# Performance work log

Measured on AMD Instinct MI355X. Metric: run time of the kernel, lower is better.

## Reference

```python
import jax, jax.numpy as jnp
import numpy as np

EPS = 1e-8  # matches torch F.cosine_similarity eps


def setup_inputs() -> dict:
    key = jax.random.key(0)
    k1, k2, k3 = jax.random.split(key, 3)
    S, B, H = 16, 512, 2048
    OGLogits = jax.random.normal(k1, (B, H), dtype=jnp.float32)
    enhancedSamplesLogits = jax.random.normal(k2, (S, B, H), dtype=jnp.float32)
    W = jax.random.normal(k3, (H, H), dtype=jnp.float32) * (1.0 / np.sqrt(H))
    b = jnp.zeros((H,), dtype=jnp.float32)
    return {"OGLogits": OGLogits, "enhancedSamplesLogits": enhancedSamplesLogits, "W": W, "b": b}


def reference(OGLogits, enhancedSamplesLogits, W, b):
    # Original torch code builds the full (S*B, B) cosine-similarity matrix and
    # keeps only the diagonal via an eye mask; mathematically that equals the
    # per-pair cosine similarity cos(enhanced[s,b], OG[b]), computed directly here.
    e_norm = jnp.linalg.norm(enhancedSamplesLogits, axis=-1)          # (S, B)
    o_norm = jnp.linalg.norm(OGLogits, axis=-1)                       # (B,)
    dots = jnp.einsum('sbh,bh->sb', enhancedSamplesLogits, OGLogits)  # (S, B)
    sims = dots / jnp.maximum(e_norm * o_norm[None, :], EPS)          # (S, B)
    weighted = enhancedSamplesLogits * sims[..., None]                # (S, B, H)
    weightedRep = weighted.mean(axis=0)                               # (B, H)
    return weightedRep @ W.T + b                                      # (B, H)
```

## Files before the change

### kernel.cpp

```cpp
#include <hip/hip_runtime.h>

#define S_DIM 16
#define B_DIM 512
#define H_DIM 2048
#define EPS 1e-8f

typedef short bf16x8 __attribute__((ext_vector_type(8)));
typedef float f32x4 __attribute__((ext_vector_type(4)));

__device__ __forceinline__ unsigned short f2bf(float f) {
    union { float f; unsigned int u; } v; v.f = f;
    unsigned int u = v.u;
    unsigned int r = (u + 0x7fffu + ((u >> 16) & 1u)) >> 16;
    return (unsigned short)r;
}

__device__ __forceinline__ float dot4(const float4& a, const float4& b) {
    return a.x*b.x + a.y*b.y + a.z*b.z + a.w*b.w;
}

__global__ __launch_bounds__(512, 4) void simwrep_kernel(
    const float* __restrict__ OG, const float* __restrict__ E,
    const float* __restrict__ W, unsigned short* __restrict__ wrep,
    unsigned short* __restrict__ Wb) {
    const int b = blockIdx.x;
    const int t = threadIdx.x;
    const int lane = t & 63;
    const int wave = t >> 6;

    __shared__ float4 ogs[512];
    __shared__ float4 buf[8][512];
    __shared__ float red[8];

    const float4* og4 = (const float4*)(OG + (size_t)b * H_DIM);
    float4 o = og4[t];
    ogs[t] = o;
    float p = dot4(o, o);
    #pragma unroll
    for (int m = 32; m >= 1; m >>= 1) p += __shfl_xor(p, m, 64);
    if (lane == 0) red[wave] = p;
    __syncthreads();
    float og2 = 0.f;
    #pragma unroll
    for (int w = 0; w < 8; ++w) og2 += red[w];
    const float onorm = sqrtf(og2);

    const float4* e4a = (const float4*)(E + ((size_t)wave * B_DIM + b) * H_DIM);
    const float4* e4b = (const float4*)(E + ((size_t)(wave + 8) * B_DIM + b) * H_DIM);
    float4 ea[8], eb[8];
    #pragma unroll
    for (int i = 0; i < 8; ++i) {
        ea[i] = e4a[i * 64 + lane];
        eb[i] = e4b[i * 64 + lane];
    }
    float da = 0.f, na = 0.f, db = 0.f, nb = 0.f;
    #pragma unroll
    for (int i = 0; i < 8; ++i) {
        float4 og = ogs[i * 64 + lane];
        da += dot4(ea[i], og);
        na += dot4(ea[i], ea[i]);
        db += dot4(eb[i], og);
        nb += dot4(eb[i], eb[i]);
    }
    #pragma unroll
    for (int m = 32; m >= 1; m >>= 1) {
        da += __shfl_xor(da, m, 64);
        na += __shfl_xor(na, m, 64);
        db += __shfl_xor(db, m, 64);
        nb += __shfl_xor(nb, m, 64);
    }
    const float sima = da / fmaxf(sqrtf(na) * onorm, EPS);
    const float simb = db / fmaxf(sqrtf(nb) * onorm, EPS);

    #pragma unroll
    for (int i = 0; i < 8; ++i) {
        float4 v;
        v.x = ea[i].x * sima + eb[i].x * simb;
        v.y = ea[i].y * sima + eb[i].y * simb;
        v.z = ea[i].z * sima + eb[i].z * simb;
        v.w = ea[i].w * sima + eb[i].w * simb;
        buf[wave][i * 64 + lane] = v;
    }
    __syncthreads();

    float4 s = buf[0][t];
    #pragma unroll
    for (int w = 1; w < 8; ++w) {
        float4 v = buf[w][t];
        s.x += v.x; s.y += v.y; s.z += v.z; s.w += v.w;
    }
    const float sc = 1.f / (float)S_DIM;
    ushort4 ob;
    ob.x = f2bf(s.x * sc); ob.y = f2bf(s.y * sc);
    ob.z = f2bf(s.z * sc); ob.w = f2bf(s.w * sc);
    ((ushort4*)wrep)[(size_t)b * (H_DIM / 4) + t] = ob;

    const float4* w4 = (const float4*)W;
    #pragma unroll
    for (int j = 0; j < 4; ++j) {
        const size_t idx = (size_t)b * 2048 + j * 512 + t;
        float4 v = w4[idx];
        ushort4 c;
        c.x = f2bf(v.x); c.y = f2bf(v.y); c.z = f2bf(v.z); c.w = f2bf(v.w);
        ((ushort4*)Wb)[idx] = c;
    }
}

__global__ __launch_bounds__(256) void gemm_kernel(
    const unsigned short* __restrict__ A, const unsigned short* __restrict__ Wb,
    const float* __restrict__ bias, float* __restrict__ out) {
    const int n0 = blockIdx.x * 32;
    const int m0 = blockIdx.y * 64;

    __shared__ unsigned short As[64][72];
    __shared__ unsigned short Ws[32][72];

    const int t = threadIdx.x;
    const int lane = t & 63;
    const int wave = t >> 6;
    const int wm = (wave & 1) * 32;
    const int wn = (wave >> 1) * 16;

    const int lrA = t >> 2, lqA = t & 3;
    const int lrB = t >> 3, lqB = t & 7;

    const unsigned short* ap = A + (size_t)(m0 + lrA) * H_DIM + lqA * 16;
    const unsigned short* bp = Wb + (size_t)(n0 + lrB) * H_DIM + lqB * 8;

    f32x4 acc0 = {0.f, 0.f, 0.f, 0.f};
    f32x4 acc1 = {0.f, 0.f, 0.f, 0.f};

    const int row = lane & 15;
    const int q = lane >> 4;

    uint4 av0 = *(const uint4*)(ap);
    uint4 av1 = *(const uint4*)(ap + 8);
    uint4 bv  = *(const uint4*)(bp);

    for (int k0 = 0; k0 < H_DIM; k0 += 64) {
        *(uint4*)&As[lrA][lqA * 16]     = av0;
        *(uint4*)&As[lrA][lqA * 16 + 8] = av1;
        *(uint4*)&Ws[lrB][lqB * 8]      = bv;
        __syncthreads();
        if (k0 + 64 < H_DIM) {
            av0 = *(const uint4*)(ap + k0 + 64);
            av1 = *(const uint4*)(ap + k0 + 72);
            bv  = *(const uint4*)(bp + k0 + 64);
        }
        #pragma unroll
        for (int ks = 0; ks < 2; ++ks) {
            bf16x8 a0 = *(const bf16x8*)&As[wm + row][ks * 32 + q * 8];
            bf16x8 a1 = *(const bf16x8*)&As[wm + 16 + row][ks * 32 + q * 8];
            bf16x8 b0 = *(const bf16x8*)&Ws[wn + row][ks * 32 + q * 8];
            acc0 = __builtin_amdgcn_mfma_f32_16x16x32_bf16(a0, b0, acc0, 0, 0, 0);
            acc1 = __builtin_amdgcn_mfma_f32_16x16x32_bf16(a1, b0, acc1, 0, 0, 0);
        }
        __syncthreads();
    }

    const int col = lane & 15;
    const float bias0 = bias[n0 + wn + col];
    #pragma unroll
    for (int r = 0; r < 4; ++r) {
        const int mr = q * 4 + r;
        float* o0 = out + (size_t)(m0 + wm + mr) * H_DIM + n0 + wn;
        float* o1 = out + (size_t)(m0 + wm + 16 + mr) * H_DIM + n0 + wn;
        o0[col] = acc0[r] + bias0;
        o1[col] = acc1[r] + bias0;
    }
}

extern "C" void kernel_launch(void* const* d_in, const int* in_sizes, int n_in,
                              void* d_out, int out_size, void* d_ws, size_t ws_size,
                              hipStream_t stream) {
    const float* OG   = (const float*)d_in[0];
    const float* E    = (const float*)d_in[1];
    const float* W    = (const float*)d_in[2];
    const float* bias = (const float*)d_in[3];
    float* out = (float*)d_out;

    unsigned short* wrep = (unsigned short*)d_ws;
    unsigned short* Wb   = wrep + (size_t)B_DIM * H_DIM;

    simwrep_kernel<<<B_DIM, 512, 0, stream>>>(OG, E, W, wrep, Wb);
    gemm_kernel<<<dim3(H_DIM / 32, B_DIM / 64), 256, 0, stream>>>(wrep, Wb, bias, out);
}
```

Measured before the change: 125.5 us.

## Pre-swizzle GEMM operands into MFMA fragment layout and drop LDS staging

The first kernel now writes the bf16 weighted representation and the converted W in a tiled layout. In that layout each 16x32 MFMA fragment sits as 64 contiguous 16-byte lanes. The GEMM then loads fragments straight from global memory into registers with one-step prefetching, with no shared-memory staging and no barriers. Each wave now computes a 32x32 tile instead of 32x16, so the grid is halved. This removes LDS traffic and syncs at the cost of relying on cache reuse for the operands that several waves share.

```diff
diff --git a/kernel.cpp b/kernel.cpp
--- a/kernel.cpp
+++ b/kernel.cpp
@@ -7,6 +7,8 @@
 
 typedef short bf16x8 __attribute__((ext_vector_type(8)));
 typedef float f32x4 __attribute__((ext_vector_type(4)));
+
+#define KT (H_DIM / 32)
 
 __device__ __forceinline__ unsigned short f2bf(float f) {
     union { float f; unsigned int u; } v; v.f = f;
@@ -21,8 +23,8 @@
 
 __global__ __launch_bounds__(512, 4) void simwrep_kernel(
     const float* __restrict__ OG, const float* __restrict__ E,
-    const float* __restrict__ W, unsigned short* __restrict__ wrep,
-    unsigned short* __restrict__ Wb) {
+    const float* __restrict__ W, unsigned short* __restrict__ wrep_sw,
+    unsigned short* __restrict__ Wb_sw) {
     const int b = blockIdx.x;
     const int t = threadIdx.x;
     const int lane = t & 63;
@@ -90,83 +92,91 @@
         s.x += v.x; s.y += v.y; s.z += v.z; s.w += v.w;
     }
     const float sc = 1.f / (float)S_DIM;
-    ushort4 ob;
-    ob.x = f2bf(s.x * sc); ob.y = f2bf(s.y * sc);
-    ob.z = f2bf(s.z * sc); ob.w = f2bf(s.w * sc);
-    ((ushort4*)wrep)[(size_t)b * (H_DIM / 4) + t] = ob;
+    {
+        const int ki = t >> 3;
+        const int quad = (t >> 1) & 3;
+        const int j0 = (t & 1) * 4;
+        const int l = (b & 15) | (quad << 4);
+        const size_t off = ((size_t)((b >> 4) * KT + ki)) * 512 + l * 8 + j0;
+        ushort4 ob;
+        ob.x = f2bf(s.x * sc); ob.y = f2bf(s.y * sc);
+        ob.z = f2bf(s.z * sc); ob.w = f2bf(s.w * sc);
+        *(ushort4*)(wrep_sw + off) = ob;
+    }
 
     const float4* w4 = (const float4*)W;
     #pragma unroll
     for (int j = 0; j < 4; ++j) {
-        const size_t idx = (size_t)b * 2048 + j * 512 + t;
+        const int n = b * 4 + j;
+        const size_t idx = (size_t)n * 512 + t;
         float4 v = w4[idx];
+        const int ki = t >> 3;
+        const int quad = (t >> 1) & 3;
+        const int j0 = (t & 1) * 4;
+        const int l = (n & 15) | (quad << 4);
+        const size_t off = ((size_t)((n >> 4) * KT + ki)) * 512 + l * 8 + j0;
         ushort4 c;
         c.x = f2bf(v.x); c.y = f2bf(v.y); c.z = f2bf(v.z); c.w = f2bf(v.w);
-        ((ushort4*)Wb)[idx] = c;
+        *(ushort4*)(Wb_sw + off) = c;
     }
 }
 
 __global__ __launch_bounds__(256) void gemm_kernel(
-    const unsigned short* __restrict__ A, const unsigned short* __restrict__ Wb,
+    const unsigned short* __restrict__ A, const unsigned short* __restrict__ Bw,
     const float* __restrict__ bias, float* __restrict__ out) {
-    const int n0 = blockIdx.x * 32;
-    const int m0 = blockIdx.y * 64;
-
-    __shared__ unsigned short As[64][72];
-    __shared__ unsigned short Ws[32][72];
-
     const int t = threadIdx.x;
     const int lane = t & 63;
     const int wave = t >> 6;
-    const int wm = (wave & 1) * 32;
-    const int wn = (wave >> 1) * 16;
+    const int mi0 = blockIdx.y * 4 + (wave & 1) * 2;
+    const int ni0 = blockIdx.x * 4 + (wave >> 1) * 2;
 
-    const int lrA = t >> 2, lqA = t & 3;
-    const int lrB = t >> 3, lqB = t & 7;
+    const bf16x8* Af = (const bf16x8*)A;
+    const bf16x8* Bf = (const bf16x8*)Bw;
+    const int a0b = mi0 * (KT * 64) + lane;
+    const int a1b = (mi0 + 1) * (KT * 64) + lane;
+    const int b0b = ni0 * (KT * 64) + lane;
+    const int b1b = (ni0 + 1) * (KT * 64) + lane;
 
-    const unsigned short* ap = A + (size_t)(m0 + lrA) * H_DIM + lqA * 16;
-    const unsigned short* bp = Wb + (size_t)(n0 + lrB) * H_DIM + lqB * 8;
+    f32x4 acc00 = {0.f, 0.f, 0.f, 0.f};
+    f32x4 acc01 = {0.f, 0.f, 0.f, 0.f};
+    f32x4 acc10 = {0.f, 0.f, 0.f, 0.f};
+    f32x4 acc11 = {0.f, 0.f, 0.f, 0.f};
 
-    f32x4 acc0 = {0.f, 0.f, 0.f, 0.f};
-    f32x4 acc1 = {0.f, 0.f, 0.f, 0.f};
+    bf16x8 a0c = Af[a0b], a1c = Af[a1b];
+    bf16x8 b0c = Bf[b0b], b1c = Bf[b1b];
 
-    const int row = lane & 15;
-    const int q = lane >> 4;
-
-    uint4 av0 = *(const uint4*)(ap);
-    uint4 av1 = *(const uint4*)(ap + 8);
-    uint4 bv  = *(const uint4*)(bp);
-
-    for (int k0 = 0; k0 < H_DIM; k0 += 64) {
-        *(uint4*)&As[lrA][lqA * 16]     = av0;
-        *(uint4*)&As[lrA][lqA * 16 + 8] = av1;
-        *(uint4*)&Ws[lrB][lqB * 8]      = bv;
-        __syncthreads();
-        if (k0 + 64 < H_DIM) {
-            av0 = *(const uint4*)(ap + k0 + 64);
-            av1 = *(const uint4*)(ap + k0 + 72);
-            bv  = *(const uint4*)(bp + k0 + 64);
-        }
-        #pragma unroll
-        for (int ks = 0; ks < 2; ++ks) {
-            bf16x8 a0 = *(const bf16x8*)&As[wm + row][ks * 32 + q * 8];
-            bf16x8 a1 = *(const bf16x8*)&As[wm + 16 + row][ks * 32 + q * 8];
-            bf16x8 b0 = *(const bf16x8*)&Ws[wn + row][ks * 32 + q * 8];
-            acc0 = __builtin_amdgcn_mfma_f32_16x16x32_bf16(a0, b0, acc0, 0, 0, 0);
-            acc1 = __builtin_amdgcn_mfma_f32_16x16x32_bf16(a1, b0, acc1, 0, 0, 0);
-        }
-        __syncthreads();
+    for (int ki = 0; ki < KT - 1; ++ki) {
+        const int nx = (ki + 1) * 64;
+        bf16x8 a0n = Af[a0b + nx];
+        bf16x8 a1n = Af[a1b + nx];
+        bf16x8 b0n = Bf[b0b + nx];
+        bf16x8 b1n = Bf[b1b + nx];
+        acc00 = __builtin_amdgcn_mfma_f32_16x16x32_bf16(a0c, b0c, acc00, 0, 0, 0);
+        acc01 = __builtin_amdgcn_mfma_f32_16x16x32_bf16(a0c, b1c, acc01, 0, 0, 0);
+        acc10 = __builtin_amdgcn_mfma_f32_16x16x32_bf16(a1c, b0c, acc10, 0, 0, 0);
+        acc11 = __builtin_amdgcn_mfma_f32_16x16x32_bf16(a1c, b1c, acc11, 0, 0, 0);
+        a0c = a0n; a1c = a1n; b0c = b0n; b1c = b1n;
     }
+    acc00 = __builtin_amdgcn_mfma_f32_16x16x32_bf16(a0c, b0c, acc00, 0, 0, 0);
+    acc01 = __builtin_amdgcn_mfma_f32_16x16x32_bf16(a0c, b1c, acc01, 0, 0, 0);
+    acc10 = __builtin_amdgcn_mfma_f32_16x16x32_bf16(a1c, b0c, acc10, 0, 0, 0);
+    acc11 = __builtin_amdgcn_mfma_f32_16x16x32_bf16(a1c, b1c, acc11, 0, 0, 0);
 
     const int col = lane & 15;
-    const float bias0 = bias[n0 + wn + col];
+    const int q = lane >> 4;
+    const int m0 = mi0 * 16;
+    const int n0 = ni0 * 16;
+    const float bias0 = bias[n0 + col];
+    const float bias1 = bias[n0 + 16 + col];
     #pragma unroll
     for (int r = 0; r < 4; ++r) {
         const int mr = q * 4 + r;
-        float* o0 = out + (size_t)(m0 + wm + mr) * H_DIM + n0 + wn;
-        float* o1 = out + (size_t)(m0 + wm + 16 + mr) * H_DIM + n0 + wn;
-        o0[col] = acc0[r] + bias0;
-        o1[col] = acc1[r] + bias0;
+        float* o0 = out + (size_t)(m0 + mr) * H_DIM + n0;
+        float* o1 = out + (size_t)(m0 + 16 + mr) * H_DIM + n0;
+        o0[col]      = acc00[r] + bias0;
+        o0[16 + col] = acc01[r] + bias1;
+        o1[col]      = acc10[r] + bias0;
+        o1[16 + col] = acc11[r] + bias1;
     }
 }
 
@@ -179,9 +189,9 @@
     const float* bias = (const float*)d_in[3];
     float* out = (float*)d_out;
 
-    unsigned short* wrep = (unsigned short*)d_ws;
-    unsigned short* Wb   = wrep + (size_t)B_DIM * H_DIM;
+    unsigned short* wrep_sw = (unsigned short*)d_ws;
+    unsigned short* Wb_sw   = wrep_sw + (size_t)B_DIM * H_DIM;
 
-    simwrep_kernel<<<B_DIM, 512, 0, stream>>>(OG, E, W, wrep, Wb);
-    gemm_kernel<<<dim3(H_DIM / 32, B_DIM / 64), 256, 0, stream>>>(wrep, Wb, bias, out);
+    simwrep_kernel<<<B_DIM, 512, 0, stream>>>(OG, E, W, wrep_sw, Wb_sw);
+    gemm_kernel<<<dim3(H_DIM / 64, B_DIM / 64), 256, 0, stream>>>(wrep_sw, Wb_sw, bias, out);
 }
```

Result: slower. 129.8 us (+3.5%).

## Use 32x32x16 MFMA with split-K across waves in GEMM kernel

Applied to the files above, without the earlier changes.

The GEMM kernel now uses one 32x32x16 bf16 MFMA per wave instead of two 16x16x32 MFMAs. The four waves are split into two M halves and two K halves of the block tile. Shared memory is re-laid out in fragment-major order so each lane reads a contiguous 16-byte fragment. The two K-halves are combined through an LDS reduction before the bias add and store. This aims for better MFMA efficiency and fewer LDS reads per flop, at the cost of an extra reduction step and half the waves sitting idle during the epilogue.

```diff
diff --git a/kernel.cpp b/kernel.cpp
--- a/kernel.cpp
+++ b/kernel.cpp
@@ -7,6 +7,7 @@
 
 typedef short bf16x8 __attribute__((ext_vector_type(8)));
 typedef float f32x4 __attribute__((ext_vector_type(4)));
+typedef float f32x16 __attribute__((ext_vector_type(16)));
 
 __device__ __forceinline__ unsigned short f2bf(float f) {
     union { float f; unsigned int u; } v; v.f = f;
@@ -112,61 +113,71 @@
     const int n0 = blockIdx.x * 32;
     const int m0 = blockIdx.y * 64;
 
-    __shared__ unsigned short As[64][72];
-    __shared__ unsigned short Ws[32][72];
+    __shared__ __align__(16) unsigned short lds[6144];
 
     const int t = threadIdx.x;
     const int lane = t & 63;
     const int wave = t >> 6;
-    const int wm = (wave & 1) * 32;
-    const int wn = (wave >> 1) * 16;
+    const int kh = wave & 1;
+    const int mh = wave >> 1;
 
-    const int lrA = t >> 2, lqA = t & 3;
-    const int lrB = t >> 3, lqB = t & 7;
+    const int ar = t >> 2;
+    const int ac = (t >> 1) & 1;
+    const int ah = t & 1;
+    const unsigned short* apg = A + (size_t)(m0 + ar) * H_DIM + ac * 1024 + ah * 16;
+    unsigned short* al0 = &lds[(((ac * 4 + ah * 2 + 0) * 64) + ar) * 8];
+    unsigned short* al1 = &lds[(((ac * 4 + ah * 2 + 1) * 64) + ar) * 8];
+    const int br = t >> 3;
+    const int bg = t & 7;
+    const unsigned short* bpg = Wb + (size_t)(n0 + br) * H_DIM + (bg >> 2) * 1024 + (bg & 3) * 8;
+    unsigned short* bl = &lds[4096 + (bg * 32 + br) * 8];
 
-    const unsigned short* ap = A + (size_t)(m0 + lrA) * H_DIM + lqA * 16;
-    const unsigned short* bp = Wb + (size_t)(n0 + lrB) * H_DIM + lqB * 8;
+    f32x16 acc = {0.f,0.f,0.f,0.f, 0.f,0.f,0.f,0.f, 0.f,0.f,0.f,0.f, 0.f,0.f,0.f,0.f};
 
-    f32x4 acc0 = {0.f, 0.f, 0.f, 0.f};
-    f32x4 acc1 = {0.f, 0.f, 0.f, 0.f};
+    const int hw = lane >> 5;
+    const int l31 = lane & 31;
 
-    const int row = lane & 15;
-    const int q = lane >> 4;
+    uint4 av0 = *(const uint4*)(apg);
+    uint4 av1 = *(const uint4*)(apg + 8);
+    uint4 bv  = *(const uint4*)(bpg);
 
-    uint4 av0 = *(const uint4*)(ap);
-    uint4 av1 = *(const uint4*)(ap + 8);
-    uint4 bv  = *(const uint4*)(bp);
-
-    for (int k0 = 0; k0 < H_DIM; k0 += 64) {
-        *(uint4*)&As[lrA][lqA * 16]     = av0;
-        *(uint4*)&As[lrA][lqA * 16 + 8] = av1;
-        *(uint4*)&Ws[lrB][lqB * 8]      = bv;
+    for (int ki = 0; ki < 32; ++ki) {
+        *(uint4*)al0 = av0;
+        *(uint4*)al1 = av1;
+        *(uint4*)bl  = bv;
         __syncthreads();
-        if (k0 + 64 < H_DIM) {
-            av0 = *(const uint4*)(ap + k0 + 64);
-            av1 = *(const uint4*)(ap + k0 + 72);
-            bv  = *(const uint4*)(bp + k0 + 64);
+        if (ki + 1 < 32) {
+            av0 = *(const uint4*)(apg + (ki + 1) * 32);
+            av1 = *(const uint4*)(apg + (ki + 1) * 32 + 8);
+            bv  = *(const uint4*)(bpg + (ki + 1) * 32);
         }
         #pragma unroll
         for (int ks = 0; ks < 2; ++ks) {
-            bf16x8 a0 = *(const bf16x8*)&As[wm + row][ks * 32 + q * 8];
-            bf16x8 a1 = *(const bf16x8*)&As[wm + 16 + row][ks * 32 + q * 8];
-            bf16x8 b0 = *(const bf16x8*)&Ws[wn + row][ks * 32 + q * 8];
-            acc0 = __builtin_amdgcn_mfma_f32_16x16x32_bf16(a0, b0, acc0, 0, 0, 0);
-            acc1 = __builtin_amdgcn_mfma_f32_16x16x32_bf16(a1, b0, acc1, 0, 0, 0);
+            const int g = kh * 4 + ks * 2 + hw;
+            bf16x8 af = *(const bf16x8*)&lds[(g * 64 + mh * 32 + l31) * 8];
+            bf16x8 bf = *(const bf16x8*)&lds[4096 + (g * 32 + l31) * 8];
+            acc = __builtin_amdgcn_mfma_f32_32x32x16_bf16(af, bf, acc, 0, 0, 0);
         }
         __syncthreads();
     }
 
-    const int col = lane & 15;
-    const float bias0 = bias[n0 + wn + col];
-    #pragma unroll
-    for (int r = 0; r < 4; ++r) {
-        const int mr = q * 4 + r;
-        float* o0 = out + (size_t)(m0 + wm + mr) * H_DIM + n0 + wn;
-        float* o1 = out + (size_t)(m0 + wm + 16 + mr) * H_DIM + n0 + wn;
-        o0[col] = acc0[r] + bias0;
-        o1[col] = acc1[r] + bias0;
+    float* red = (float*)lds;
+    if (kh == 1) {
+        #pragma unroll
+        for (int r = 0; r < 16; ++r) {
+            const int orow = (r & 3) + 8 * (r >> 2) + 4 * hw;
+            red[mh * 1024 + orow * 32 + l31] = acc[r];
+        }
+    }
+    __syncthreads();
+    if (kh == 0) {
+        const float b0 = bias[n0 + l31];
+        #pragma unroll
+        for (int r = 0; r < 16; ++r) {
+            const int orow = (r & 3) + 8 * (r >> 2) + 4 * hw;
+            out[(size_t)(m0 + mh * 32 + orow) * H_DIM + n0 + l31] =
+                acc[r] + red[mh * 1024 + orow * 32 + l31] + b0;
+        }
     }
 }
 
```

Measured after the change: 130.8 us. 4.2% more time.
